# Kernel tuning notes

Measured on AMD Instinct MI355X. Metric: run time of the kernel, lower is better.

Reference implementation:

```python
import jax, jax.numpy as jnp
import numpy as np

NUM_HEADS = 8
LN_EPS = 1e-5
COS_EPS = 1e-8


def setup_inputs() -> dict:
    key = jax.random.key(0)
    ks = jax.random.split(key, 16)
    B, S, H, C = 16, 4096, 768, 64
    std = 0.02
    f32 = jnp.float32
    return {
        "hidden_states": jax.random.normal(ks[0], (B, S, H), f32),
        "concept_embeddings": jax.random.normal(ks[1], (C, H), f32),
        "Wq": jax.random.normal(ks[2], (H, H), f32) * std,
        "bq": jnp.zeros((H,), f32),
        "Wk": jax.random.normal(ks[3], (H, H), f32) * std,
        "bk": jnp.zeros((H,), f32),
        "Wv": jax.random.normal(ks[4], (H, H), f32) * std,
        "bv": jnp.zeros((H,), f32),
        "Wo": jax.random.normal(ks[5], (H, H), f32) * std,
        "bo": jnp.zeros((H,), f32),
        "Wg1": jax.random.normal(ks[6], (3 * H, H), f32) * std,
        "bg1": jnp.zeros((H,), f32),
        "Wg2": jax.random.normal(ks[7], (H, 1), f32) * std,
        "bg2": jnp.zeros((1,), f32),
        "ln_g": jnp.ones((H,), f32),
        "ln_b": jnp.zeros((H,), f32),
    }


def reference(hidden_states, concept_embeddings, Wq, bq, Wk, bk, Wv, bv,
              Wo, bo, Wg1, bg1, Wg2, bg2, ln_g, ln_b):
    B, S, H = hidden_states.shape
    C = concept_embeddings.shape[0]
    NH = NUM_HEADS
    HD = H // NH

    # QKV projections; concepts are shared across the batch
    Q = (hidden_states @ Wq + bq).reshape(B, S, NH, HD)      # [B,S,NH,HD]
    K = (concept_embeddings @ Wk + bk).reshape(C, NH, HD)    # [C,NH,HD]
    V = (concept_embeddings @ Wv + bv).reshape(C, NH, HD)

    scores = jnp.einsum('bshd,chd->bhsc', Q, K) / (HD ** 0.5)  # [B,NH,S,C]
    attn = jax.nn.softmax(scores, axis=-1)  # dropout is eval-mode identity
    context = jnp.einsum('bhsc,chd->bshd', attn, V).reshape(B, S, H)
    context = context @ Wo + bo

    # content relevance: cosine sim of mean-pooled text vs mean-pooled concepts
    text_pooled = hidden_states.mean(axis=1)          # [B,H]
    concept_pooled = concept_embeddings.mean(axis=0)  # [H] (same for all batch)
    num = text_pooled @ concept_pooled                # [B]
    den = jnp.maximum(jnp.linalg.norm(text_pooled, axis=-1), COS_EPS) * \
          jnp.maximum(jnp.linalg.norm(concept_pooled), COS_EPS)
    relevance = num / den                             # [B]
    rel_feat = jnp.broadcast_to(relevance[:, None, None], (B, S, H))

    gate_in = jnp.concatenate([hidden_states, context, rel_feat], axis=-1)  # [B,S,3H]
    gate = jax.nn.sigmoid(jax.nn.relu(gate_in @ Wg1 + bg1) @ Wg2 + bg2)     # [B,S,1]

    out = hidden_states + gate * context
    mu = out.mean(axis=-1, keepdims=True)
    var = out.var(axis=-1, keepdims=True)
    out = (out - mu) / jnp.sqrt(var + LN_EPS) * ln_g + ln_b

    attn_avg = attn.mean(axis=1)  # [B,S,C] for XAI
    return out, attn_avg
```

## Files before the change

### kernel.cpp

```cpp
#include <hip/hip_runtime.h>

typedef __attribute__((ext_vector_type(8))) short bf16x8;
typedef __attribute__((ext_vector_type(4))) float f32x4;
typedef unsigned short u16;

#define MFMA(a,b,c) __builtin_amdgcn_mfma_f32_16x16x32_bf16((a),(b),(c),0,0,0)

__device__ __forceinline__ short f2bf(float f){
  union { float f; unsigned u; } v; v.f = f;
  unsigned r = v.u + 0x7FFFu + ((v.u >> 16) & 1u);
  return (short)(r >> 16);
}
__device__ __forceinline__ float bf2f(short s){
  union { unsigned u; float f; } v; v.u = ((unsigned)(unsigned short)s) << 16; return v.f;
}
__device__ __forceinline__ bf16x8 pack8(f32x4 x, f32x4 y){
  bf16x8 r;
  r[0]=f2bf(x[0]); r[1]=f2bf(x[1]); r[2]=f2bf(x[2]); r[3]=f2bf(x[3]);
  r[4]=f2bf(y[0]); r[5]=f2bf(y[1]); r[6]=f2bf(y[2]); r[7]=f2bf(y[3]);
  return r;
}
__device__ __forceinline__ int pch(int c, int row){ return (c & ~7) | ((c & 7) ^ (row & 7)); }

__device__ __forceinline__ void gload16(void* lp, const void* gp){
  __builtin_amdgcn_global_load_lds((const __attribute__((address_space(1))) unsigned*)gp,
                                   (__attribute__((address_space(3))) unsigned*)lp, 16, 0, 0);
}
__device__ __forceinline__ void stWB(short* buf, const short* img, int half, int w, int lane){
  const char* gp = (const char*)img;
  #pragma unroll
  for (int it=0; it<4; ++it){
    int id = it*256 + w*64 + lane; int r = id>>3, c = id&7;
    gload16((char*)buf + it*4096 + w*1024, gp + r*256 + half*128 + c*16);
  }
}
__device__ __forceinline__ void stA256(short* buf, const u16* rowb, int kstep, int w, int lane){
  int tid = w*64 + lane;
  #pragma unroll
  for (int it=0; it<4; ++it){
    int id = it*512 + tid; int r = id>>3, c = id&7;
    gload16((char*)buf + it*8192 + w*1024, rowb + (size_t)r*1536 + (kstep*8 + c)*8);
  }
}
__device__ __forceinline__ void stB256(short* buf, const short* img, int half, int w, int lane){
  int tid = w*64 + lane;
  #pragma unroll
  for (int it=0; it<4; ++it){
    int id = it*512 + tid; int r = id>>3, c = id&7;
    gload16((char*)buf + it*8192 + w*1024,
            img + (size_t)(r>>7)*98304 + (size_t)(r&127)*128 + half*64 + c*8);
  }
}

__global__ __launch_bounds__(256) void prep1(const float* __restrict__ ce,
    const float* __restrict__ Wk, const float* __restrict__ bk,
    const float* __restrict__ Wv, const float* __restrict__ bv,
    const float* __restrict__ Wg1, short* __restrict__ Kc, short* __restrict__ VT,
    short* __restrict__ WaI, short* __restrict__ WbI){
  __shared__ float smemf[8704];
  int b = blockIdx.x, tid = threadIdx.x;
  if (b < 96){
    float* sh = smemf;
    int jt = b / 8, cg = b % 8;
    int j = jt*64 + (tid & 63);
    int cl = tid >> 6;
    for (int i = tid; i < 8*768; i += 256){
      int c2 = i / 768; int h = i - c2*768;
      sh[c2*768 + h] = ce[(size_t)(cg*8+c2)*768 + h];
    }
    __syncthreads();
    float aK0=0.f, aV0=0.f, aK1=0.f, aV1=0.f;
    #pragma unroll 4
    for (int h=0; h<768; ++h){
      float wk = Wk[(size_t)h*768 + j];
      float wv = Wv[(size_t)h*768 + j];
      float x0 = sh[(cl*2)*768 + h], x1 = sh[(cl*2+1)*768 + h];
      aK0 += x0*wk; aV0 += x0*wv;
      aK1 += x1*wk; aV1 += x1*wv;
    }
    float bkj = bk[j], bvj = bv[j];
    int c0 = cg*8 + cl*2;
    Kc[(size_t)c0*768 + j]     = f2bf(aK0 + bkj);
    Kc[(size_t)(c0+1)*768 + j] = f2bf(aK1 + bkj);
    VT[(size_t)j*64 + c0]      = f2bf(aV0 + bvj);
    VT[(size_t)j*64 + c0+1]    = f2bf(aV1 + bvj);
  } else {
    short* lt = (short*)smemf;
    int blk = b - 96;
    int mat = blk / 36, t = blk % 36, kt = t / 6, jt = t % 6;
    const float* src = (mat==0)? Wg1 : (Wg1 + (size_t)768*768);
    short* dst = (mat==0)? WaI : WbI;
    #pragma unroll
    for (int it=0; it<16; ++it){
      int kl = it*8 + (tid>>5);
      int jl = (tid&31)*4;
      f32x4 v = *(const f32x4*)&src[(size_t)(kt*128+kl)*768 + jt*128 + jl];
      lt[(jl+0)*136+kl]=f2bf(v[0]); lt[(jl+1)*136+kl]=f2bf(v[1]);
      lt[(jl+2)*136+kl]=f2bf(v[2]); lt[(jl+3)*136+kl]=f2bf(v[3]);
    }
    __syncthreads();
    size_t base = (size_t)(jt*6 + kt)*16384;
    #pragma unroll
    for (int cc=0; cc<8; ++cc){
      int ci = cc*256 + tid;
      int jl = ci >> 4, sc = ci & 15;
      int kkb = ((sc ^ (jl & 7)) << 3);
      bf16x8 v = *(const bf16x8*)&lt[jl*136 + kkb];
      *(bf16x8*)&dst[base + (size_t)jl*128 + sc*8] = v;
    }
  }
}

__global__ __launch_bounds__(256) void prep2(const float* __restrict__ Wg1,
    const float* __restrict__ ce, const float* __restrict__ bq,
    const short* __restrict__ Kc, const float* __restrict__ Wq,
    const float* __restrict__ Wo, const short* __restrict__ VT,
    float* __restrict__ wg1c, float* __restrict__ cp, float* __restrict__ sbias,
    short* __restrict__ WeffI, short* __restrict__ VWoI){
  __shared__ float smemf[9984];
  int b = blockIdx.x, tid = threadIdx.x;
  if (b < 17){
    float* red = smemf;
    if (b < 12){
      int j = b*64 + (tid & 63);
      int kq = tid >> 6;
      float s = 0.f;
      for (int r=0; r<192; ++r)
        s += Wg1[(size_t)(1536 + kq*192 + r)*768 + j];
      red[kq*64 + (tid&63)] = s;
      __syncthreads();
      if (tid < 64) wg1c[b*64+tid] = red[tid]+red[64+tid]+red[128+tid]+red[192+tid];
    } else if (b < 15){
      int h = (b-12)*256 + tid;
      float s = 0.f;
      #pragma unroll
      for (int c2=0; c2<64; ++c2) s += ce[(size_t)c2*768 + h];
      cp[h] = s * (1.f/64.f);
    } else {
      int hc = (b-15)*256 + tid;
      int h = hc >> 6, c = hc & 63;
      float s = 0.f;
      #pragma unroll
      for (int j=0; j<96; ++j)
        s += bq[h*96+j] * bf2f(Kc[(size_t)c*768 + h*96 + j]);
      sbias[hc] = s * 0.10206207262f;
    }
  } else if (b < 65){
    short* KA = (short*)smemf;
    short* WB = KA + 6656;
    int e = b - 17;
    int h = e / 6, kt = e % 6;
    const int lane = tid & 63, w = tid >> 6, l15 = lane & 15, g = lane >> 4;
    #pragma unroll
    for (int it=0; it<3; ++it){
      int i = it*256 + tid;
      int c = i / 12, cb = i % 12;
      *(bf16x8*)&KA[c*104 + cb*8] = *(const bf16x8*)&Kc[(size_t)c*768 + h*96 + cb*8];
    }
    #pragma unroll
    for (int it=0; it<12; ++it){
      int i = it*256 + tid;
      int d = i / 24, q = i % 24;
      f32x4 v = *(const f32x4*)&Wq[(size_t)(kt*128+d)*768 + h*96 + q*4];
      WB[d*104 + q*4+0]=f2bf(v[0]); WB[d*104 + q*4+1]=f2bf(v[1]);
      WB[d*104 + q*4+2]=f2bf(v[2]); WB[d*104 + q*4+3]=f2bf(v[3]);
    }
    __syncthreads();
    f32x4 acc[4][2];
    #pragma unroll
    for (int i=0;i<4;++i){ acc[i][0]=(f32x4){0,0,0,0}; acc[i][1]=(f32x4){0,0,0,0}; }
    #pragma unroll
    for (int ks=0; ks<3; ++ks){
      bf16x8 a[4], bb[2];
      #pragma unroll
      for (int mf=0; mf<4; ++mf) a[mf] = *(const bf16x8*)&KA[(mf*16+l15)*104 + ks*32+g*8];
      #pragma unroll
      for (int nf=0; nf<2; ++nf) bb[nf] = *(const bf16x8*)&WB[(w*32+nf*16+l15)*104 + ks*32+g*8];
      #pragma unroll
      for (int mf=0; mf<4; ++mf)
        #pragma unroll
        for (int nf=0; nf<2; ++nf)
          acc[mf][nf] = MFMA(a[mf], bb[nf], acc[mf][nf]);
    }
    size_t base = (size_t)((h>>1)*6 + kt)*16384;
    #pragma unroll
    for (int mf=0; mf<4; ++mf)
      #pragma unroll
      for (int nf=0; nf<2; ++nf)
        #pragma unroll
        for (int r=0; r<4; ++r){
          int c = mf*16 + g*4 + r;
          int d = w*32 + nf*16 + l15;
          int hcl = (h&1)*64 + c;
          WeffI[base + (size_t)hcl*128 + (((d>>3)^(hcl&7))<<3) + (d&7)] = f2bf(acc[mf][nf][r] * 0.10206207262f);
        }
  } else {
    short* WoT = (short*)smemf;
    short* VA  = WoT + 13312;
    int e = b - 65;
    int h = e / 6, dt = e % 6;
    const int lane = tid & 63, w = tid >> 6, l15 = lane & 15, g = lane >> 4;
    #pragma unroll
    for (int it=0; it<12; ++it){
      int i = it*256 + tid;
      int j = i / 32, qd = i % 32;
      f32x4 v = *(const f32x4*)&Wo[(size_t)(h*96+j)*768 + dt*128 + qd*4];
      WoT[(qd*4+0)*104 + j]=f2bf(v[0]); WoT[(qd*4+1)*104 + j]=f2bf(v[1]);
      WoT[(qd*4+2)*104 + j]=f2bf(v[2]); WoT[(qd*4+3)*104 + j]=f2bf(v[3]);
    }
    #pragma unroll
    for (int it=0; it<3; ++it){
      int i = it*256 + tid;
      int j = i / 8, cb = i % 8;
      bf16x8 v = *(const bf16x8*)&VT[(size_t)(h*96+j)*64 + cb*8];
      #pragma unroll
      for (int x=0; x<8; ++x) VA[(cb*8+x)*104 + j] = v[x];
    }
    __syncthreads();
    f32x4 acc[2][4];
    #pragma unroll
    for (int i=0;i<2;++i)
      #pragma unroll
      for (int j=0;j<4;++j) acc[i][j]=(f32x4){0,0,0,0};
    #pragma unroll
    for (int ks=0; ks<3; ++ks){
      bf16x8 a[2], bb[4];
      #pragma unroll
      for (int mf=0; mf<2; ++mf) a[mf] = *(const bf16x8*)&WoT[(w*32+mf*16+l15)*104 + ks*32+g*8];
      #pragma unroll
      for (int nf=0; nf<4; ++nf) bb[nf] = *(const bf16x8*)&VA[(nf*16+l15)*104 + ks*32+g*8];
      #pragma unroll
      for (int mf=0; mf<2; ++mf)
        #pragma unroll
        for (int nf=0; nf<4; ++nf)
          acc[mf][nf] = MFMA(a[mf], bb[nf], acc[mf][nf]);
    }
    size_t base = (size_t)(dt*4 + (h>>1))*16384;
    #pragma unroll
    for (int mf=0; mf<2; ++mf)
      #pragma unroll
      for (int nf=0; nf<4; ++nf)
        #pragma unroll
        for (int r=0; r<4; ++r){
          int d = w*32 + mf*16 + g*4 + r;
          int c = nf*16 + l15;
          int hcl = (h&1)*64 + c;
          VWoI[base + (size_t)d*128 + (((hcl>>3)^(d&7))<<3) + (hcl&7)] = f2bf(acc[mf][nf][r]);
        }
  }
}

__global__ __launch_bounds__(384) void prep_hs(const float* __restrict__ hs,
                                               float* __restrict__ outp, float* __restrict__ tpp){
  __shared__ float csum[4][768];
  int tid = threadIdx.x;
  int c = tid % 96, rg = tid / 96;
  size_t r0 = (size_t)blockIdx.x * 128;
  u16* holes = (u16*)outp;
  float s[8];
  #pragma unroll
  for (int j=0;j<8;++j) s[j]=0.f;
  #pragma unroll 4
  for (int i=0; i<32; ++i){
    size_t row = r0 + rg*32 + i;
    const float* p = hs + row*768 + c*8;
    f32x4 x = __builtin_nontemporal_load((const f32x4*)p);
    f32x4 y = __builtin_nontemporal_load((const f32x4*)(p+4));
    *(bf16x8*)&holes[row*1536 + pch(c,(int)row)*8] = pack8(x,y);
    #pragma unroll
    for (int j=0;j<4;++j){ s[j]+=x[j]; s[4+j]+=y[j]; }
  }
  #pragma unroll
  for (int j=0;j<8;++j) csum[rg][c*8+j] = s[j];
  __syncthreads();
  for (int cc=tid; cc<768; cc+=384)
    tpp[(size_t)blockIdx.x*768 + cc] = csum[0][cc]+csum[1][cc]+csum[2][cc]+csum[3][cc];
}

__global__ void pool23(const float* __restrict__ tpp, const float* __restrict__ cp,
                       float* __restrict__ rel){
  int b = blockIdx.x;
  float a=0.f, n1=0.f, n2=0.f;
  for (int h = threadIdx.x; h < 768; h += 256){
    float s = 0.f;
    #pragma unroll
    for (int k=0; k<32; ++k) s += tpp[((size_t)b*32 + k)*768 + h];
    s *= (1.f/4096.f);
    float c = cp[h];
    a += s*c; n1 += s*s; n2 += c*c;
  }
  #pragma unroll
  for (int m=1; m<64; m<<=1){ a+=__shfl_xor(a,m); n1+=__shfl_xor(n1,m); n2+=__shfl_xor(n2,m); }
  __shared__ float r3[3][4];
  int w = threadIdx.x >> 6;
  if ((threadIdx.x & 63) == 0){ r3[0][w]=a; r3[1][w]=n1; r3[2][w]=n2; }
  __syncthreads();
  if (threadIdx.x == 0){
    float A = r3[0][0]+r3[0][1]+r3[0][2]+r3[0][3];
    float N1= r3[1][0]+r3[1][1]+r3[1][2]+r3[1][3];
    float N2= r3[2][0]+r3[2][1]+r3[2][2]+r3[2][3];
    rel[b] = A / (fmaxf(sqrtf(N1),1e-8f) * fmaxf(sqrtf(N2),1e-8f));
  }
}

__global__ void __launch_bounds__(512)
__attribute__((amdgpu_waves_per_eu(2, 2))) gs256(const short* __restrict__ WeffI,
    const float* __restrict__ sbias, float* outp){
  extern __shared__ char lds[];
  short* A0 = (short*)lds;
  short* A1 = (short*)(lds + 32768);
  short* B0 = (short*)(lds + 65536);
  short* B1 = (short*)(lds + 98304);
  const int tid = threadIdx.x, lane = tid & 63, w = tid >> 6;
  const int l15 = lane & 15, g = lane >> 4;
  const int bid = blockIdx.x;
  const int nb = (bid >> 3) & 1, mt = (bid >> 4)*8 + (bid & 7);
  const int wm = w & 1, wn = w >> 1;
  const size_t t0 = (size_t)mt*256;
  u16* holes = (u16*)outp;
  const u16* h1p = holes + t0*1536;
  const short* Wimg = WeffI + (size_t)(nb*2)*98304;
  f32x4 acc[8][4];
  #pragma unroll
  for (int i=0;i<8;++i)
    #pragma unroll
    for (int j=0;j<4;++j) acc[i][j]=(f32x4){0.f,0.f,0.f,0.f};
  stA256(A0, h1p, 0, w, lane);
  stB256(B0, Wimg, 0, w, lane);
  __syncthreads();
  #pragma unroll
  for (int ks2=0; ks2<12; ++ks2){
    const short* Ac = (ks2&1)? A1 : A0;
    const short* Bc = (ks2&1)? B1 : B0;
    short* An = (ks2&1)? A0 : A1;
    short* Bn = (ks2&1)? B0 : B1;
    if (ks2<11){
      stA256(An, h1p, ks2+1, w, lane);
      stB256(Bn, Wimg + (size_t)((ks2+1)>>1)*16384, (ks2+1)&1, w, lane);
    }
    #pragma unroll
    for (int ks=0; ks<2; ++ks){
      bf16x8 a[8], b[4];
      #pragma unroll
      for (int mf=0; mf<8; ++mf){ int r = wm*128+mf*16+l15; a[mf] = *(const bf16x8*)&Ac[r*64 + (((ks*4+g)^(r&7))<<3)]; }
      #pragma unroll
      for (int nf=0; nf<4; ++nf){ int r = wn*64+nf*16+l15; b[nf] = *(const bf16x8*)&Bc[r*64 + (((ks*4+g)^(r&7))<<3)]; }
      #pragma unroll
      for (int mf=0; mf<8; ++mf)
        #pragma unroll
        for (int nf=0; nf<4; ++nf)
          acc[mf][nf] = MFMA(a[mf], b[nf], acc[mf][nf]);
    }
    __syncthreads();
  }
  #pragma unroll
  for (int mf=0; mf<8; ++mf)
    #pragma unroll
    for (int r=0; r<4; ++r){
      float v[4];
      #pragma unroll
      for (int nf=0; nf<4; ++nf)
        v[nf] = acc[mf][nf][r] + sbias[nb*256 + wn*64 + nf*16 + l15];
      float m = fmaxf(fmaxf(v[0],v[1]), fmaxf(v[2],v[3]));
      m = fmaxf(m,__shfl_xor(m,1)); m = fmaxf(m,__shfl_xor(m,2));
      m = fmaxf(m,__shfl_xor(m,4)); m = fmaxf(m,__shfl_xor(m,8));
      float e[4]; float s = 0.f;
      #pragma unroll
      for (int nf=0; nf<4; ++nf){ e[nf] = __expf(v[nf]-m); s += e[nf]; }
      s += __shfl_xor(s,1); s += __shfl_xor(s,2); s += __shfl_xor(s,4); s += __shfl_xor(s,8);
      float inv = 1.f/s;
      int grow = wm*128 + mf*16 + g*4 + r;
      #pragma unroll
      for (int nf=0; nf<4; ++nf){
        int col = nb*256 + wn*64 + nf*16 + l15;
        holes[(t0+grow)*1536 + 768 + pch(col>>3, grow)*8 + (col&7)] = (u16)f2bf(e[nf]*inv);
      }
    }
}

__global__ __launch_bounds__(256) void gvwo(const short* __restrict__ VWoI,
                                            const float* __restrict__ bo, float* outp){
  __shared__ short B0[8192], B1[8192];
  const int tid = threadIdx.x, lane = tid & 63, w = tid >> 6;
  const int l15 = lane & 15, g = lane >> 4;
  const size_t t0 = (size_t)blockIdx.x * 64;
  const int arow = w*16 + l15;
  const int drow = w*16 + g*4;
  u16* holes = (u16*)outp;
  bf16x8 af[16];
  #pragma unroll
  for (int kk=0; kk<16; ++kk){
    int kc = kk*4 + g;
    af[kk] = *(const bf16x8*)&holes[(t0+arow)*1536 + 768 + pch(kc, arow)*8];
  }
  stWB(B0, VWoI, 0, w, lane);
  {
    float s0[8], s1[8];
    #pragma unroll
    for (int j=0;j<8;++j){ s0[j]=0.f; s1[j]=0.f; }
    #pragma unroll
    for (int kk=0; kk<16; kk+=2)
      #pragma unroll
      for (int j=0;j<8;++j) s0[j] += bf2f(af[kk][j]);
    #pragma unroll
    for (int kk=1; kk<16; kk+=2)
      #pragma unroll
      for (int j=0;j<8;++j) s1[j] += bf2f(af[kk][j]);
    float* ap = &outp[(size_t)50331648 + (size_t)(t0+arow)*64];
    f32x4 o;
    #pragma unroll
    for (int j=0;j<4;++j) o[j] = s0[j]*0.125f;
    __builtin_nontemporal_store(o, (f32x4*)(ap + g*8));
    #pragma unroll
    for (int j=0;j<4;++j) o[j] = s0[4+j]*0.125f;
    __builtin_nontemporal_store(o, (f32x4*)(ap + g*8 + 4));
    #pragma unroll
    for (int j=0;j<4;++j) o[j] = s1[j]*0.125f;
    __builtin_nontemporal_store(o, (f32x4*)(ap + (4+g)*8));
    #pragma unroll
    for (int j=0;j<4;++j) o[j] = s1[4+j]*0.125f;
    __builtin_nontemporal_store(o, (f32x4*)(ap + (4+g)*8 + 4));
  }
  __syncthreads();
  #pragma unroll 1
  for (int nb=0; nb<6; ++nb){
    f32x4 acc[8];
    #pragma unroll
    for (int i=0;i<8;++i) acc[i]=(f32x4){0.f,0.f,0.f,0.f};
    #pragma unroll
    for (int ks2=0; ks2<8; ++ks2){
      const short* Bc = (ks2&1)? B1 : B0;
      short* Bn = (ks2&1)? B0 : B1;
      if (ks2<7)       stWB(Bn, VWoI + (size_t)(nb*4 + ((ks2+1)>>1))*16384, (ks2+1)&1, w, lane);
      else if (nb<5)   stWB(Bn, VWoI + (size_t)((nb+1)*4)*16384, 0, w, lane);
      #pragma unroll
      for (int ks=0; ks<2; ++ks){
        bf16x8 a = af[ks2*2 + ks];
        #pragma unroll
        for (int nf=0; nf<8; ++nf){
          int br = nf*16 + l15;
          bf16x8 b = *(const bf16x8*)&Bc[br*64 + (((ks*4+g)^(br&7))<<3)];
          acc[nf] = MFMA(a, b, acc[nf]);
        }
      }
      __syncthreads();
    }
    #pragma unroll
    for (int nf=0; nf<8; ++nf)
      #pragma unroll
      for (int r=0; r<4; ++r){
        int row = drow + r;
        int col = nb*128 + nf*16 + l15;
        float v = acc[nf][r] + bo[col];
        holes[(t0+row)*1536 + 768 + pch(col>>3, row)*8 + (col&7)] = (u16)f2bf(v);
      }
  }
}

__global__ void __launch_bounds__(512)
__attribute__((amdgpu_waves_per_eu(2, 2))) gate_mm(const short* __restrict__ WaI,
    const short* __restrict__ WbI, const float* __restrict__ bg1,
    const float* __restrict__ wg1c, const float* __restrict__ Wg2,
    const float* __restrict__ rel, float* __restrict__ gpart, float* outp){
  extern __shared__ char lds[];
  short* A0 = (short*)lds;
  short* A1 = (short*)(lds + 32768);
  short* B0 = (short*)(lds + 65536);
  short* B1 = (short*)(lds + 98304);
  const int tid = threadIdx.x, lane = tid & 63, w = tid >> 6;
  const int l15 = lane & 15, g = lane >> 4;
  const int bid = blockIdx.x;
  const int nb = (bid >> 3) % 3, mt = (bid/24)*8 + (bid & 7);
  const int wm = w & 1, wn = w >> 1;
  const size_t t0 = (size_t)mt*256;
  const float relb = rel[t0 >> 12];
  u16* holes = (u16*)outp;
  const u16* h1p = holes + t0*1536;
  const u16* h2p = h1p + 768;
  f32x4 acc[8][4];
  #pragma unroll
  for (int i=0;i<8;++i)
    #pragma unroll
    for (int j=0;j<4;++j) acc[i][j]=(f32x4){0.f,0.f,0.f,0.f};
  stA256(A0, h1p, 0, w, lane);
  stB256(B0, WaI + (size_t)(nb*2)*98304, 0, w, lane);
  __syncthreads();
  #pragma unroll 1
  for (int pass=0; pass<2; ++pass){
    const short* Wimg = pass ? (WbI + (size_t)(nb*2)*98304) : (WaI + (size_t)(nb*2)*98304);
    const u16* Ap = pass ? h2p : h1p;
    #pragma unroll
    for (int ks2=0; ks2<12; ++ks2){
      const short* Ac = (ks2&1)? A1 : A0;
      const short* Bc = (ks2&1)? B1 : B0;
      short* An = (ks2&1)? A0 : A1;
      short* Bn = (ks2&1)? B0 : B1;
      if (ks2<11){
        stA256(An, Ap, ks2+1, w, lane);
        stB256(Bn, Wimg + (size_t)((ks2+1)>>1)*16384, (ks2+1)&1, w, lane);
      } else if (pass==0){
        stA256(An, h2p, 0, w, lane);
        stB256(Bn, WbI + (size_t)(nb*2)*98304, 0, w, lane);
      }
      #pragma unroll
      for (int ks=0; ks<2; ++ks){
        bf16x8 a[8], b[4];
        #pragma unroll
        for (int mf=0; mf<8; ++mf){ int r = wm*128+mf*16+l15; a[mf] = *(const bf16x8*)&Ac[r*64 + (((ks*4+g)^(r&7))<<3)]; }
        #pragma unroll
        for (int nf=0; nf<4; ++nf){ int r = wn*64+nf*16+l15; b[nf] = *(const bf16x8*)&Bc[r*64 + (((ks*4+g)^(r&7))<<3)]; }
        #pragma unroll
        for (int mf=0; mf<8; ++mf)
          #pragma unroll
          for (int nf=0; nf<4; ++nf)
            acc[mf][nf] = MFMA(a[mf], b[nf], acc[mf][nf]);
      }
      __syncthreads();
    }
  }
  float gp[8][4];
  #pragma unroll
  for (int mf=0; mf<8; ++mf)
    #pragma unroll
    for (int r=0; r<4; ++r) gp[mf][r]=0.f;
  #pragma unroll
  for (int mf=0; mf<8; ++mf)
    #pragma unroll
    for (int nf=0; nf<4; ++nf)
      #pragma unroll
      for (int r=0; r<4; ++r){
        int col = nb*256 + wn*64 + nf*16 + l15;
        gp[mf][r] += fmaxf(acc[mf][nf][r] + bg1[col] + relb*wg1c[col], 0.f) * Wg2[col];
      }
  #pragma unroll
  for (int mf=0; mf<8; ++mf)
    #pragma unroll
    for (int r=0; r<4; ++r){
      float v = gp[mf][r];
      v += __shfl_xor(v,1); v += __shfl_xor(v,2); v += __shfl_xor(v,4); v += __shfl_xor(v,8);
      gp[mf][r] = v;
    }
  float* gred = (float*)lds;
  if (l15 == 0)
    #pragma unroll
    for (int mf=0; mf<8; ++mf)
      #pragma unroll
      for (int r=0; r<4; ++r)
        gred[wn*256 + wm*128 + mf*16 + g*4 + r] = gp[mf][r];
  __syncthreads();
  if (tid < 256)
    gpart[(size_t)nb*65536 + t0 + tid] = gred[tid] + gred[256+tid] + gred[512+tid] + gred[768+tid];
}

__global__ __launch_bounds__(256) void lnk(const float* __restrict__ gpart,
    const float* __restrict__ bg2, const float* __restrict__ lng,
    const float* __restrict__ lnb, float* outp){
  const int tid = threadIdx.x, lane = tid & 63, w = tid >> 6;
  u16* holes = (u16*)outp;
  const float bg2v = bg2[0];
  #pragma unroll 1
  for (int i=0; i<8; ++i){
    int row = blockIdx.x*32 + w*8 + i;
    float gsum = bg2v;
    #pragma unroll
    for (int nb2=0; nb2<3; ++nb2) gsum += gpart[(size_t)nb2*65536 + row];
    float gg = 1.f/(1.f + __expf(-gsum));
    int c1 = lane, c2 = 64 + (lane & 31);
    size_t rb = (size_t)row*1536;
    bf16x8 hv1 = __builtin_nontemporal_load((const bf16x8*)&holes[rb + pch(c1,row)*8]);
    bf16x8 ov1 = __builtin_nontemporal_load((const bf16x8*)&holes[rb + 768 + pch(c1,row)*8]);
    bf16x8 hv2 = __builtin_nontemporal_load((const bf16x8*)&holes[rb + pch(c2,row)*8]);
    bf16x8 ov2 = __builtin_nontemporal_load((const bf16x8*)&holes[rb + 768 + pch(c2,row)*8]);
    float x1[8], x2[8];
    float sum=0.f, sq=0.f;
    #pragma unroll
    for (int j=0;j<8;++j){ float x = bf2f(hv1[j]) + gg*bf2f(ov1[j]); x1[j]=x; sum+=x; sq+=x*x; }
    if (lane < 32){
      #pragma unroll
      for (int j=0;j<8;++j){ float x = bf2f(hv2[j]) + gg*bf2f(ov2[j]); x2[j]=x; sum+=x; sq+=x*x; }
    }
    #pragma unroll
    for (int m=1; m<64; m<<=1){ sum += __shfl_xor(sum,m); sq += __shfl_xor(sq,m); }
    float mu = sum * (1.f/768.f);
    float var = sq * (1.f/768.f) - mu*mu;
    float rs = rsqrtf(var + 1e-5f);
    {
      f32x4 ga = *(const f32x4*)&lng[c1*8], gb = *(const f32x4*)&lng[c1*8+4];
      f32x4 ba = *(const f32x4*)&lnb[c1*8], bb = *(const f32x4*)&lnb[c1*8+4];
      f32x4 o0, o1;
      #pragma unroll
      for (int j=0;j<4;++j){ o0[j] = (x1[j]-mu)*rs*ga[j]+ba[j]; o1[j] = (x1[4+j]-mu)*rs*gb[j]+bb[j]; }
      __builtin_nontemporal_store(o0, (f32x4*)&outp[(size_t)row*768 + c1*8]);
      __builtin_nontemporal_store(o1, (f32x4*)&outp[(size_t)row*768 + c1*8 + 4]);
    }
    if (lane < 32){
      f32x4 ga = *(const f32x4*)&lng[c2*8], gb = *(const f32x4*)&lng[c2*8+4];
      f32x4 ba = *(const f32x4*)&lnb[c2*8], bb = *(const f32x4*)&lnb[c2*8+4];
      f32x4 o0, o1;
      #pragma unroll
      for (int j=0;j<4;++j){ o0[j] = (x2[j]-mu)*rs*ga[j]+ba[j]; o1[j] = (x2[4+j]-mu)*rs*gb[j]+bb[j]; }
      __builtin_nontemporal_store(o0, (f32x4*)&outp[(size_t)row*768 + c2*8]);
      __builtin_nontemporal_store(o1, (f32x4*)&outp[(size_t)row*768 + c2*8 + 4]);
    }
  }
}

extern "C" void kernel_launch(void* const* d_in, const int* in_sizes, int n_in,
                              void* d_out, int out_size, void* d_ws, size_t ws_size,
                              hipStream_t stream) {
  (void)in_sizes; (void)n_in; (void)out_size; (void)ws_size;
  const float* hs  = (const float*)d_in[0];
  const float* ce  = (const float*)d_in[1];
  const float* Wq  = (const float*)d_in[2];
  const float* bq  = (const float*)d_in[3];
  const float* Wk  = (const float*)d_in[4];
  const float* bk  = (const float*)d_in[5];
  const float* Wv  = (const float*)d_in[6];
  const float* bv  = (const float*)d_in[7];
  const float* Wo  = (const float*)d_in[8];
  const float* bo  = (const float*)d_in[9];
  const float* Wg1 = (const float*)d_in[10];
  const float* bg1 = (const float*)d_in[11];
  const float* Wg2 = (const float*)d_in[12];
  const float* bg2 = (const float*)d_in[13];
  const float* lng = (const float*)d_in[14];
  const float* lnb = (const float*)d_in[15];
  char* ws = (char*)d_ws;
  short* WeffI = (short*)(ws + 0);
  short* VWoI  = (short*)(ws + 1179648);
  short* WaI   = (short*)(ws + 2359296);
  short* WbI   = (short*)(ws + 3538944);
  short* Kc    = (short*)(ws + 4718592);
  short* VT    = (short*)(ws + 4816896);
  float* wg1c  = (float*)(ws + 4915200);
  float* cp    = (float*)(ws + 4918272);
  float* rel   = (float*)(ws + 4970496);
  float* tpp   = (float*)(ws + 4970752);
  float* gpart = (float*)(ws + 4970752);
  float* sbias = (float*)(ws + 6543616);
  float* outp  = (float*)d_out;

  prep1   <<<168, 256, 0, stream>>>(ce, Wk, bk, Wv, bv, Wg1, Kc, VT, WaI, WbI);
  prep2   <<<113, 256, 0, stream>>>(Wg1, ce, bq, Kc, Wq, Wo, VT, wg1c, cp, sbias, WeffI, VWoI);
  prep_hs <<<512, 384, 0, stream>>>(hs, outp, tpp);
  pool23  <<<16,  256, 0, stream>>>(tpp, cp, rel);
  hipFuncSetAttribute(reinterpret_cast<const void*>(gs256),
                      hipFuncAttributeMaxDynamicSharedMemorySize, 131072);
  gs256   <<<512, 512, 131072, stream>>>(WeffI, sbias, outp);
  gvwo    <<<1024,256, 0, stream>>>(VWoI, bo, outp);
  hipFuncSetAttribute(reinterpret_cast<const void*>(gate_mm),
                      hipFuncAttributeMaxDynamicSharedMemorySize, 131072);
  gate_mm <<<768, 512, 131072, stream>>>(WaI, WbI, bg1, wg1c, Wg2, rel, gpart, outp);
  lnk     <<<2048,256, 0, stream>>>(gpart, bg2, lng, lnb, outp);
}
```

Measured before the change: 491.1 us.

## Merge pool23 into prep2, move cp into prep1, widen gvwo to two column blocks

Moves the concept mean-pooling into prep1 and folds the relevance reduction (formerly pool23) into prep2, which now runs after prep_hs. This removes one kernel launch. Separately, gvwo now processes two 128-column output blocks per pass with dual double-buffered LDS tiles, halving the outer loop trips and barriers. That doubles gvwo's LDS use to 64KB per block and its accumulator registers, which may reduce occupancy.

```diff
diff --git a/kernel.cpp b/kernel.cpp
--- a/kernel.cpp
+++ b/kernel.cpp
@@ -56,7 +56,7 @@
     const float* __restrict__ Wk, const float* __restrict__ bk,
     const float* __restrict__ Wv, const float* __restrict__ bv,
     const float* __restrict__ Wg1, short* __restrict__ Kc, short* __restrict__ VT,
-    short* __restrict__ WaI, short* __restrict__ WbI){
+    short* __restrict__ WaI, short* __restrict__ WbI, float* __restrict__ cp){
   __shared__ float smemf[8704];
   int b = blockIdx.x, tid = threadIdx.x;
   if (b < 96){
@@ -84,7 +84,7 @@
     Kc[(size_t)(c0+1)*768 + j] = f2bf(aK1 + bkj);
     VT[(size_t)j*64 + c0]      = f2bf(aV0 + bvj);
     VT[(size_t)j*64 + c0+1]    = f2bf(aV1 + bvj);
-  } else {
+  } else if (b < 168){
     short* lt = (short*)smemf;
     int blk = b - 96;
     int mat = blk / 36, t = blk % 36, kt = t / 6, jt = t % 6;
@@ -108,145 +108,12 @@
       bf16x8 v = *(const bf16x8*)&lt[jl*136 + kkb];
       *(bf16x8*)&dst[base + (size_t)jl*128 + sc*8] = v;
     }
-  }
-}
-
-__global__ __launch_bounds__(256) void prep2(const float* __restrict__ Wg1,
-    const float* __restrict__ ce, const float* __restrict__ bq,
-    const short* __restrict__ Kc, const float* __restrict__ Wq,
-    const float* __restrict__ Wo, const short* __restrict__ VT,
-    float* __restrict__ wg1c, float* __restrict__ cp, float* __restrict__ sbias,
-    short* __restrict__ WeffI, short* __restrict__ VWoI){
-  __shared__ float smemf[9984];
-  int b = blockIdx.x, tid = threadIdx.x;
-  if (b < 17){
-    float* red = smemf;
-    if (b < 12){
-      int j = b*64 + (tid & 63);
-      int kq = tid >> 6;
-      float s = 0.f;
-      for (int r=0; r<192; ++r)
-        s += Wg1[(size_t)(1536 + kq*192 + r)*768 + j];
-      red[kq*64 + (tid&63)] = s;
-      __syncthreads();
-      if (tid < 64) wg1c[b*64+tid] = red[tid]+red[64+tid]+red[128+tid]+red[192+tid];
-    } else if (b < 15){
-      int h = (b-12)*256 + tid;
-      float s = 0.f;
-      #pragma unroll
-      for (int c2=0; c2<64; ++c2) s += ce[(size_t)c2*768 + h];
-      cp[h] = s * (1.f/64.f);
-    } else {
-      int hc = (b-15)*256 + tid;
-      int h = hc >> 6, c = hc & 63;
-      float s = 0.f;
-      #pragma unroll
-      for (int j=0; j<96; ++j)
-        s += bq[h*96+j] * bf2f(Kc[(size_t)c*768 + h*96 + j]);
-      sbias[hc] = s * 0.10206207262f;
-    }
-  } else if (b < 65){
-    short* KA = (short*)smemf;
-    short* WB = KA + 6656;
-    int e = b - 17;
-    int h = e / 6, kt = e % 6;
-    const int lane = tid & 63, w = tid >> 6, l15 = lane & 15, g = lane >> 4;
-    #pragma unroll
-    for (int it=0; it<3; ++it){
-      int i = it*256 + tid;
-      int c = i / 12, cb = i % 12;
-      *(bf16x8*)&KA[c*104 + cb*8] = *(const bf16x8*)&Kc[(size_t)c*768 + h*96 + cb*8];
-    }
-    #pragma unroll
-    for (int it=0; it<12; ++it){
-      int i = it*256 + tid;
-      int d = i / 24, q = i % 24;
-      f32x4 v = *(const f32x4*)&Wq[(size_t)(kt*128+d)*768 + h*96 + q*4];
-      WB[d*104 + q*4+0]=f2bf(v[0]); WB[d*104 + q*4+1]=f2bf(v[1]);
-      WB[d*104 + q*4+2]=f2bf(v[2]); WB[d*104 + q*4+3]=f2bf(v[3]);
-    }
-    __syncthreads();
-    f32x4 acc[4][2];
-    #pragma unroll
-    for (int i=0;i<4;++i){ acc[i][0]=(f32x4){0,0,0,0}; acc[i][1]=(f32x4){0,0,0,0}; }
-    #pragma unroll
-    for (int ks=0; ks<3; ++ks){
-      bf16x8 a[4], bb[2];
-      #pragma unroll
-      for (int mf=0; mf<4; ++mf) a[mf] = *(const bf16x8*)&KA[(mf*16+l15)*104 + ks*32+g*8];
-      #pragma unroll
-      for (int nf=0; nf<2; ++nf) bb[nf] = *(const bf16x8*)&WB[(w*32+nf*16+l15)*104 + ks*32+g*8];
-      #pragma unroll
-      for (int mf=0; mf<4; ++mf)
-        #pragma unroll
-        for (int nf=0; nf<2; ++nf)
-          acc[mf][nf] = MFMA(a[mf], bb[nf], acc[mf][nf]);
-    }
-    size_t base = (size_t)((h>>1)*6 + kt)*16384;
-    #pragma unroll
-    for (int mf=0; mf<4; ++mf)
-      #pragma unroll
-      for (int nf=0; nf<2; ++nf)
-        #pragma unroll
-        for (int r=0; r<4; ++r){
-          int c = mf*16 + g*4 + r;
-          int d = w*32 + nf*16 + l15;
-          int hcl = (h&1)*64 + c;
-          WeffI[base + (size_t)hcl*128 + (((d>>3)^(hcl&7))<<3) + (d&7)] = f2bf(acc[mf][nf][r] * 0.10206207262f);
-        }
   } else {
-    short* WoT = (short*)smemf;
-    short* VA  = WoT + 13312;
-    int e = b - 65;
-    int h = e / 6, dt = e % 6;
-    const int lane = tid & 63, w = tid >> 6, l15 = lane & 15, g = lane >> 4;
-    #pragma unroll
-    for (int it=0; it<12; ++it){
-      int i = it*256 + tid;
-      int j = i / 32, qd = i % 32;
-      f32x4 v = *(const f32x4*)&Wo[(size_t)(h*96+j)*768 + dt*128 + qd*4];
-      WoT[(qd*4+0)*104 + j]=f2bf(v[0]); WoT[(qd*4+1)*104 + j]=f2bf(v[1]);
-      WoT[(qd*4+2)*104 + j]=f2bf(v[2]); WoT[(qd*4+3)*104 + j]=f2bf(v[3]);
-    }
-    #pragma unroll
-    for (int it=0; it<3; ++it){
-      int i = it*256 + tid;
-      int j = i / 8, cb = i % 8;
-      bf16x8 v = *(const bf16x8*)&VT[(size_t)(h*96+j)*64 + cb*8];
-      #pragma unroll
-      for (int x=0; x<8; ++x) VA[(cb*8+x)*104 + j] = v[x];
-    }
-    __syncthreads();
-    f32x4 acc[2][4];
-    #pragma unroll
-    for (int i=0;i<2;++i)
-      #pragma unroll
-      for (int j=0;j<4;++j) acc[i][j]=(f32x4){0,0,0,0};
-    #pragma unroll
-    for (int ks=0; ks<3; ++ks){
-      bf16x8 a[2], bb[4];
-      #pragma unroll
-      for (int mf=0; mf<2; ++mf) a[mf] = *(const bf16x8*)&WoT[(w*32+mf*16+l15)*104 + ks*32+g*8];
-      #pragma unroll
-      for (int nf=0; nf<4; ++nf) bb[nf] = *(const bf16x8*)&VA[(nf*16+l15)*104 + ks*32+g*8];
-      #pragma unroll
-      for (int mf=0; mf<2; ++mf)
-        #pragma unroll
-        for (int nf=0; nf<4; ++nf)
-          acc[mf][nf] = MFMA(a[mf], bb[nf], acc[mf][nf]);
-    }
-    size_t base = (size_t)(dt*4 + (h>>1))*16384;
-    #pragma unroll
-    for (int mf=0; mf<2; ++mf)
-      #pragma unroll
-      for (int nf=0; nf<4; ++nf)
-        #pragma unroll
-        for (int r=0; r<4; ++r){
-          int d = w*32 + mf*16 + g*4 + r;
-          int c = nf*16 + l15;
-          int hcl = (h&1)*64 + c;
-          VWoI[base + (size_t)d*128 + (((hcl>>3)^(d&7))<<3) + (hcl&7)] = f2bf(acc[mf][nf][r]);
-        }
+    int h = (b-168)*256 + tid;
+    float s = 0.f;
+    #pragma unroll
+    for (int c2=0; c2<64; ++c2) s += ce[(size_t)c2*768 + h];
+    cp[h] = s * (1.f/64.f);
   }
 }
 
@@ -277,29 +144,158 @@
     tpp[(size_t)blockIdx.x*768 + cc] = csum[0][cc]+csum[1][cc]+csum[2][cc]+csum[3][cc];
 }
 
-__global__ void pool23(const float* __restrict__ tpp, const float* __restrict__ cp,
-                       float* __restrict__ rel){
-  int b = blockIdx.x;
-  float a=0.f, n1=0.f, n2=0.f;
-  for (int h = threadIdx.x; h < 768; h += 256){
+__global__ __launch_bounds__(256) void prep2(const float* __restrict__ Wg1,
+    const float* __restrict__ ce, const float* __restrict__ bq,
+    const short* __restrict__ Kc, const float* __restrict__ Wq,
+    const float* __restrict__ Wo, const short* __restrict__ VT,
+    const float* __restrict__ tpp, const float* __restrict__ cp,
+    float* __restrict__ wg1c, float* __restrict__ sbias,
+    short* __restrict__ WeffI, short* __restrict__ VWoI, float* __restrict__ rel){
+  __shared__ float smemf[9984];
+  int b = blockIdx.x, tid = threadIdx.x;
+  if (b < 12){
+    float* red = smemf;
+    int j = b*64 + (tid & 63);
+    int kq = tid >> 6;
     float s = 0.f;
-    #pragma unroll
-    for (int k=0; k<32; ++k) s += tpp[((size_t)b*32 + k)*768 + h];
-    s *= (1.f/4096.f);
-    float c = cp[h];
-    a += s*c; n1 += s*s; n2 += c*c;
-  }
-  #pragma unroll
-  for (int m=1; m<64; m<<=1){ a+=__shfl_xor(a,m); n1+=__shfl_xor(n1,m); n2+=__shfl_xor(n2,m); }
-  __shared__ float r3[3][4];
-  int w = threadIdx.x >> 6;
-  if ((threadIdx.x & 63) == 0){ r3[0][w]=a; r3[1][w]=n1; r3[2][w]=n2; }
-  __syncthreads();
-  if (threadIdx.x == 0){
-    float A = r3[0][0]+r3[0][1]+r3[0][2]+r3[0][3];
-    float N1= r3[1][0]+r3[1][1]+r3[1][2]+r3[1][3];
-    float N2= r3[2][0]+r3[2][1]+r3[2][2]+r3[2][3];
-    rel[b] = A / (fmaxf(sqrtf(N1),1e-8f) * fmaxf(sqrtf(N2),1e-8f));
+    for (int r=0; r<192; ++r)
+      s += Wg1[(size_t)(1536 + kq*192 + r)*768 + j];
+    red[kq*64 + (tid&63)] = s;
+    __syncthreads();
+    if (tid < 64) wg1c[b*64+tid] = red[tid]+red[64+tid]+red[128+tid]+red[192+tid];
+  } else if (b < 14){
+    int hc = (b-12)*256 + tid;
+    int h = hc >> 6, c = hc & 63;
+    float s = 0.f;
+    #pragma unroll
+    for (int j=0; j<96; ++j)
+      s += bq[h*96+j] * bf2f(Kc[(size_t)c*768 + h*96 + j]);
+    sbias[hc] = s * 0.10206207262f;
+  } else if (b < 62){
+    short* KA = (short*)smemf;
+    short* WB = KA + 6656;
+    int e = b - 14;
+    int h = e / 6, kt = e % 6;
+    const int lane = tid & 63, w = tid >> 6, l15 = lane & 15, g = lane >> 4;
+    #pragma unroll
+    for (int it=0; it<3; ++it){
+      int i = it*256 + tid;
+      int c = i / 12, cb = i % 12;
+      *(bf16x8*)&KA[c*104 + cb*8] = *(const bf16x8*)&Kc[(size_t)c*768 + h*96 + cb*8];
+    }
+    #pragma unroll
+    for (int it=0; it<12; ++it){
+      int i = it*256 + tid;
+      int d = i / 24, q = i % 24;
+      f32x4 v = *(const f32x4*)&Wq[(size_t)(kt*128+d)*768 + h*96 + q*4];
+      WB[d*104 + q*4+0]=f2bf(v[0]); WB[d*104 + q*4+1]=f2bf(v[1]);
+      WB[d*104 + q*4+2]=f2bf(v[2]); WB[d*104 + q*4+3]=f2bf(v[3]);
+    }
+    __syncthreads();
+    f32x4 acc[4][2];
+    #pragma unroll
+    for (int i=0;i<4;++i){ acc[i][0]=(f32x4){0,0,0,0}; acc[i][1]=(f32x4){0,0,0,0}; }
+    #pragma unroll
+    for (int ks=0; ks<3; ++ks){
+      bf16x8 a[4], bb[2];
+      #pragma unroll
+      for (int mf=0; mf<4; ++mf) a[mf] = *(const bf16x8*)&KA[(mf*16+l15)*104 + ks*32+g*8];
+      #pragma unroll
+      for (int nf=0; nf<2; ++nf) bb[nf] = *(const bf16x8*)&WB[(w*32+nf*16+l15)*104 + ks*32+g*8];
+      #pragma unroll
+      for (int mf=0; mf<4; ++mf)
+        #pragma unroll
+        for (int nf=0; nf<2; ++nf)
+          acc[mf][nf] = MFMA(a[mf], bb[nf], acc[mf][nf]);
+    }
+    size_t base = (size_t)((h>>1)*6 + kt)*16384;
+    #pragma unroll
+    for (int mf=0; mf<4; ++mf)
+      #pragma unroll
+      for (int nf=0; nf<2; ++nf)
+        #pragma unroll
+        for (int r=0; r<4; ++r){
+          int c = mf*16 + g*4 + r;
+          int d = w*32 + nf*16 + l15;
+          int hcl = (h&1)*64 + c;
+          WeffI[base + (size_t)hcl*128 + (((d>>3)^(hcl&7))<<3) + (d&7)] = f2bf(acc[mf][nf][r] * 0.10206207262f);
+        }
+  } else if (b < 110){
+    short* WoT = (short*)smemf;
+    short* VA  = WoT + 13312;
+    int e = b - 62;
+    int h = e / 6, dt = e % 6;
+    const int lane = tid & 63, w = tid >> 6, l15 = lane & 15, g = lane >> 4;
+    #pragma unroll
+    for (int it=0; it<12; ++it){
+      int i = it*256 + tid;
+      int j = i / 32, qd = i % 32;
+      f32x4 v = *(const f32x4*)&Wo[(size_t)(h*96+j)*768 + dt*128 + qd*4];
+      WoT[(qd*4+0)*104 + j]=f2bf(v[0]); WoT[(qd*4+1)*104 + j]=f2bf(v[1]);
+      WoT[(qd*4+2)*104 + j]=f2bf(v[2]); WoT[(qd*4+3)*104 + j]=f2bf(v[3]);
+    }
+    #pragma unroll
+    for (int it=0; it<3; ++it){
+      int i = it*256 + tid;
+      int j = i / 8, cb = i % 8;
+      bf16x8 v = *(const bf16x8*)&VT[(size_t)(h*96+j)*64 + cb*8];
+      #pragma unroll
+      for (int x=0; x<8; ++x) VA[(cb*8+x)*104 + j] = v[x];
+    }
+    __syncthreads();
+    f32x4 acc[2][4];
+    #pragma unroll
+    for (int i=0;i<2;++i)
+      #pragma unroll
+      for (int j=0;j<4;++j) acc[i][j]=(f32x4){0,0,0,0};
+    #pragma unroll
+    for (int ks=0; ks<3; ++ks){
+      bf16x8 a[2], bb[4];
+      #pragma unroll
+      for (int mf=0; mf<2; ++mf) a[mf] = *(const bf16x8*)&WoT[(w*32+mf*16+l15)*104 + ks*32+g*8];
+      #pragma unroll
+      for (int nf=0; nf<4; ++nf) bb[nf] = *(const bf16x8*)&VA[(nf*16+l15)*104 + ks*32+g*8];
+      #pragma unroll
+      for (int mf=0; mf<2; ++mf)
+        #pragma unroll
+        for (int nf=0; nf<4; ++nf)
+          acc[mf][nf] = MFMA(a[mf], bb[nf], acc[mf][nf]);
+    }
+    size_t base = (size_t)(dt*4 + (h>>1))*16384;
+    #pragma unroll
+    for (int mf=0; mf<2; ++mf)
+      #pragma unroll
+      for (int nf=0; nf<4; ++nf)
+        #pragma unroll
+        for (int r=0; r<4; ++r){
+          int d = w*32 + mf*16 + g*4 + r;
+          int c = nf*16 + l15;
+          int hcl = (h&1)*64 + c;
+          VWoI[base + (size_t)d*128 + (((hcl>>3)^(d&7))<<3) + (hcl&7)] = f2bf(acc[mf][nf][r]);
+        }
+  } else {
+    int bb2 = b - 110;
+    float a=0.f, n1=0.f, n2=0.f;
+    for (int h = tid; h < 768; h += 256){
+      float s = 0.f;
+      #pragma unroll
+      for (int k=0; k<32; ++k) s += tpp[((size_t)bb2*32 + k)*768 + h];
+      s *= (1.f/4096.f);
+      float c = cp[h];
+      a += s*c; n1 += s*s; n2 += c*c;
+    }
+    #pragma unroll
+    for (int m=1; m<64; m<<=1){ a+=__shfl_xor(a,m); n1+=__shfl_xor(n1,m); n2+=__shfl_xor(n2,m); }
+    float* r3 = smemf;
+    int w = tid >> 6;
+    if ((tid & 63) == 0){ r3[0*4+w]=a; r3[1*4+w]=n1; r3[2*4+w]=n2; }
+    __syncthreads();
+    if (tid == 0){
+      float A = r3[0]+r3[1]+r3[2]+r3[3];
+      float N1= r3[4]+r3[5]+r3[6]+r3[7];
+      float N2= r3[8]+r3[9]+r3[10]+r3[11];
+      rel[bb2] = A / (fmaxf(sqrtf(N1),1e-8f) * fmaxf(sqrtf(N2),1e-8f));
+    }
   }
 }
 
@@ -380,7 +376,7 @@
 
 __global__ __launch_bounds__(256) void gvwo(const short* __restrict__ VWoI,
                                             const float* __restrict__ bo, float* outp){
-  __shared__ short B0[8192], B1[8192];
+  __shared__ short B0a[8192], B1a[8192], B0b[8192], B1b[8192];
   const int tid = threadIdx.x, lane = tid & 63, w = tid >> 6;
   const int l15 = lane & 15, g = lane >> 4;
   const size_t t0 = (size_t)blockIdx.x * 64;
@@ -393,7 +389,8 @@
     int kc = kk*4 + g;
     af[kk] = *(const bf16x8*)&holes[(t0+arow)*1536 + 768 + pch(kc, arow)*8];
   }
-  stWB(B0, VWoI, 0, w, lane);
+  stWB(B0a, VWoI, 0, w, lane);
+  stWB(B0b, VWoI + (size_t)4*16384, 0, w, lane);
   {
     float s0[8], s1[8];
     #pragma unroll
@@ -423,24 +420,34 @@
   }
   __syncthreads();
   #pragma unroll 1
-  for (int nb=0; nb<6; ++nb){
-    f32x4 acc[8];
-    #pragma unroll
-    for (int i=0;i<8;++i) acc[i]=(f32x4){0.f,0.f,0.f,0.f};
+  for (int nb2=0; nb2<3; ++nb2){
+    f32x4 accA[8], accB[8];
+    #pragma unroll
+    for (int i=0;i<8;++i){ accA[i]=(f32x4){0.f,0.f,0.f,0.f}; accB[i]=(f32x4){0.f,0.f,0.f,0.f}; }
+    const short* imgA = VWoI + (size_t)(nb2*2)*4*16384;
+    const short* imgB = VWoI + (size_t)(nb2*2+1)*4*16384;
     #pragma unroll
     for (int ks2=0; ks2<8; ++ks2){
-      const short* Bc = (ks2&1)? B1 : B0;
-      short* Bn = (ks2&1)? B0 : B1;
-      if (ks2<7)       stWB(Bn, VWoI + (size_t)(nb*4 + ((ks2+1)>>1))*16384, (ks2+1)&1, w, lane);
-      else if (nb<5)   stWB(Bn, VWoI + (size_t)((nb+1)*4)*16384, 0, w, lane);
+      const short* Bca = (ks2&1)? B1a : B0a;
+      const short* Bcb = (ks2&1)? B1b : B0b;
+      short* Bna = (ks2&1)? B0a : B1a;
+      short* Bnb = (ks2&1)? B0b : B1b;
+      if (ks2<7){
+        stWB(Bna, imgA + (size_t)((ks2+1)>>1)*16384, (ks2+1)&1, w, lane);
+        stWB(Bnb, imgB + (size_t)((ks2+1)>>1)*16384, (ks2+1)&1, w, lane);
+      } else if (nb2<2){
+        stWB(Bna, VWoI + (size_t)((nb2+1)*2)*4*16384, 0, w, lane);
+        stWB(Bnb, VWoI + (size_t)((nb2+1)*2+1)*4*16384, 0, w, lane);
+      }
       #pragma unroll
       for (int ks=0; ks<2; ++ks){
         bf16x8 a = af[ks2*2 + ks];
         #pragma unroll
         for (int nf=0; nf<8; ++nf){
           int br = nf*16 + l15;
-          bf16x8 b = *(const bf16x8*)&Bc[br*64 + (((ks*4+g)^(br&7))<<3)];
-          acc[nf] = MFMA(a, b, acc[nf]);
+          int off = br*64 + (((ks*4+g)^(br&7))<<3);
+          accA[nf] = MFMA(a, *(const bf16x8*)&Bca[off], accA[nf]);
+          accB[nf] = MFMA(a, *(const bf16x8*)&Bcb[off], accB[nf]);
         }
       }
       __syncthreads();
@@ -450,9 +457,10 @@
       #pragma unroll
       for (int r=0; r<4; ++r){
         int row = drow + r;
-        int col = nb*128 + nf*16 + l15;
-        float v = acc[nf][r] + bo[col];
-        holes[(t0+row)*1536 + 768 + pch(col>>3, row)*8 + (col&7)] = (u16)f2bf(v);
+        int colA = (nb2*2)*128 + nf*16 + l15;
+        int colB = (nb2*2+1)*128 + nf*16 + l15;
+        holes[(t0+row)*1536 + 768 + pch(colA>>3, row)*8 + (colA&7)] = (u16)f2bf(accA[nf][r] + bo[colA]);
+        holes[(t0+row)*1536 + 768 + pch(colB>>3, row)*8 + (colB&7)] = (u16)f2bf(accB[nf][r] + bo[colB]);
       }
   }
 }
@@ -640,10 +648,10 @@
   float* sbias = (float*)(ws + 6543616);
   float* outp  = (float*)d_out;
 
-  prep1   <<<168, 256, 0, stream>>>(ce, Wk, bk, Wv, bv, Wg1, Kc, VT, WaI, WbI);
-  prep2   <<<113, 256, 0, stream>>>(Wg1, ce, bq, Kc, Wq, Wo, VT, wg1c, cp, sbias, WeffI, VWoI);
+  prep1   <<<171, 256, 0, stream>>>(ce, Wk, bk, Wv, bv, Wg1, Kc, VT, WaI, WbI, cp);
   prep_hs <<<512, 384, 0, stream>>>(hs, outp, tpp);
-  pool23  <<<16,  256, 0, stream>>>(tpp, cp, rel);
+  prep2   <<<126, 256, 0, stream>>>(Wg1, ce, bq, Kc, Wq, Wo, VT, tpp, cp,
+                                    wg1c, sbias, WeffI, VWoI, rel);
   hipFuncSetAttribute(reinterpret_cast<const void*>(gs256),
                       hipFuncAttributeMaxDynamicSharedMemorySize, 131072);
   gs256   <<<512, 512, 131072, stream>>>(WeffI, sbias, outp);
```

Result: slower. 523.0 us (+6.5%).
